# Kernel optimization log

Hardware: AMD Instinct MI355X
Metric: run time of the kernel (lower is better)

## Reference

```python
import jax, jax.numpy as jnp
import numpy as np
from jax import lax

ALIGNED_H = 7
ALIGNED_W = 7
SPATIAL_SCALE = 0.125
B, C, H, W = 4, 512, 96, 96
R = 512
IMG = 768  # image resolution (features are image/8)


def setup_inputs() -> dict:
    key = jax.random.key(0)
    k1, k2, k3, k4, k5, k6 = jax.random.split(key, 6)
    features = jax.random.normal(k1, (B, C, H, W), dtype=jnp.float32)
    # realistic rois: [batch_idx, x1, y1, x2, y2] in image coordinates
    bi = jax.random.randint(k2, (R,), 0, B).astype(jnp.float32)
    cx = jax.random.uniform(k3, (R,), minval=32.0, maxval=float(IMG - 32))
    cy = jax.random.uniform(k4, (R,), minval=32.0, maxval=float(IMG - 32))
    bw = jax.random.uniform(k5, (R,), minval=16.0, maxval=256.0)
    bh = jax.random.uniform(k6, (R,), minval=16.0, maxval=256.0)
    x1 = jnp.clip(cx - bw / 2, 0.0, IMG - 1.0)
    x2 = jnp.clip(cx + bw / 2, 0.0, IMG - 1.0)
    y1 = jnp.clip(cy - bh / 2, 0.0, IMG - 1.0)
    y2 = jnp.clip(cy + bh / 2, 0.0, IMG - 1.0)
    rois = jnp.stack([bi, x1, y1, x2, y2], axis=1)
    return {"features": features, "rois": rois}


def _roi_align_ada(features, rois, ah, aw, scale):
    """RoIAlignAda: per output pixel, average of a 3x3 adaptive-stride grid of
    bilinear samples centered at the bin point (RT-MDNet ROIAlignAdaForward)."""
    b, c, h, w = features.shape
    r = rois.shape[0]
    batch_ind = rois[:, 0].astype(jnp.int32)
    x1 = rois[:, 1] * scale
    y1 = rois[:, 2] * scale
    x2 = rois[:, 3] * scale
    y2 = rois[:, 4] * scale
    roi_w = jnp.maximum(x2 - x1, 0.0)
    roi_h = jnp.maximum(y2 - y1, 0.0)
    bin_h = roi_h / (ah - 1.0)  # [R]
    bin_w = roi_w / (aw - 1.0)
    ph = jnp.arange(ah, dtype=jnp.float32)
    pw = jnp.arange(aw, dtype=jnp.float32)
    hc = y1[:, None] + ph[None, :] * bin_h[:, None]  # [R, AH] bin centers
    wc = x1[:, None] + pw[None, :] * bin_w[:, None]  # [R, AW]
    stride_h = jnp.maximum(1.0, jnp.round(bin_h / 3.0))  # [R]
    stride_w = jnp.maximum(1.0, jnp.round(bin_w / 3.0))

    center_ok = ((hc >= 0) & (hc < h))[:, :, None] & ((wc >= 0) & (wc < w))[:, None, :]  # [R,AH,AW]

    # flatten spatial for gathers: [B*H*W, C]
    f = features.transpose(0, 2, 3, 1).reshape(b * h * w, c)
    base = batch_ind[:, None, None] * (h * w)  # [R,1,1]

    acc = jnp.zeros((r, ah, aw, c), dtype=features.dtype)
    cnt = jnp.zeros((r, ah, aw), dtype=features.dtype)
    for sh in (-1.0, 0.0, 1.0):
        for sw in (-1.0, 0.0, 1.0):
            ch = hc + sh * stride_h[:, None]  # [R,AH]
            cw = wc + sw * stride_w[:, None]  # [R,AW]
            valid = ((ch >= 0) & (ch < h))[:, :, None] & ((cw >= 0) & (cw < w))[:, None, :]
            hs = jnp.clip(jnp.floor(ch), 0.0, h - 2.0)
            ws = jnp.clip(jnp.floor(cw), 0.0, w - 2.0)
            hr = (ch - hs)[:, :, None]  # [R,AH,1]
            wr = (cw - ws)[:, None, :] * jnp.ones((r, ah, aw), features.dtype)[:, :1, :1]  # broadcast helper
            wr = (cw - ws)[:, None, :]  # [R,1,AW]
            hsi = hs.astype(jnp.int32)[:, :, None]  # [R,AH,1]
            wsi = ws.astype(jnp.int32)[:, None, :]  # [R,1,AW]
            ul = base + hsi * w + wsi  # [R,AH,AW]
            v = (f[ul] * ((1.0 - hr) * (1.0 - wr))[..., None]
                 + f[ul + 1] * ((1.0 - hr) * wr)[..., None]
                 + f[ul + w] * (hr * (1.0 - wr))[..., None]
                 + f[ul + w + 1] * (hr * wr)[..., None])  # [R,AH,AW,C]
            acc = acc + jnp.where(valid[..., None], v, 0.0)
            cnt = cnt + valid.astype(features.dtype)

    out = jnp.where(center_ok[..., None], acc / jnp.maximum(cnt, 1.0)[..., None], 0.0)
    return out.transpose(0, 3, 1, 2)  # [R, C, AH, AW]


def reference(features, rois):
    x = _roi_align_ada(features, rois, ALIGNED_H + 4, ALIGNED_W + 4, SPATIAL_SCALE)  # [R,C,11,11]
    # fused 3x3 stride-2 max pool -> [R, C, 5, 5]
    out = lax.reduce_window(x, -jnp.inf, lax.max,
                            window_dimensions=(1, 1, 3, 3),
                            window_strides=(1, 1, 2, 2),
                            padding='VALID')
    return out
```

## Files before the change

### kernel.cpp

```cpp
#include <hip/hip_runtime.h>
#include <stdint.h>

typedef unsigned short u16;
typedef unsigned int   u32;

#define Bn 4
#define Cc 512
#define Hh 96
#define Ww 96
#define HWc (Hh*Ww)
#define AH 11
#define Rr 512
#define CP (Cc/2)

__device__ __forceinline__ u16 f2bf(float f){
  u32 u = __float_as_uint(f);
  u += 0x7fffu + ((u>>16)&1u);
  return (u16)(u>>16);
}
__device__ __forceinline__ u32 pk2(float a, float b){
  return (u32)f2bf(a) | ((u32)f2bf(b)<<16);
}

__global__ __launch_bounds__(256)
void transpose_kernel(const float* __restrict__ in, u32* __restrict__ out,
                      const float* __restrict__ rois, int* __restrict__ idx){
  __shared__ u32 tile[128*64];
  const int t = threadIdx.x;
  const int hw0 = blockIdx.x*128, c0 = blockIdx.y*128, b = blockIdx.z;
  {
    const int q = t & 31, cp0 = t >> 5;
    const float* ib = in + ((size_t)(b*Cc + c0))*HWc + hw0 + 4*q;
    #pragma unroll
    for (int p=0;p<8;++p){
      const int cp = cp0 + p*8;
      const float* pa = ib + (size_t)(2*cp)*HWc;
      float4 A = *(const float4*)pa;
      float4 B = *(const float4*)(pa + HWc);
      const int cs = cp ^ q;
      tile[(4*q+0)*64 + cs] = pk2(A.x,B.x);
      tile[(4*q+1)*64 + cs] = pk2(A.y,B.y);
      tile[(4*q+2)*64 + cs] = pk2(A.z,B.z);
      tile[(4*q+3)*64 + cs] = pk2(A.w,B.w);
    }
  }
  __syncthreads();
  {
    const int l = t & 63, wv = t >> 6;
    const int rsub = l >> 4, q = l & 15;
    u32* ob = out + ((size_t)b*HWc + hw0)*CP + (c0>>1);
    #pragma unroll
    for (int k=0;k<8;++k){
      const int hw = wv*32 + k*4 + rsub;
      const int s  = hw >> 2;
      const int m  = s & 3;
      const u32* tp = &tile[hw*64 + ((4*q) ^ (s & ~3))];
      uint4 R = *(const uint4*)tp;
      uint4 W;
      if      (m==0) W = R;
      else if (m==1) W = make_uint4(R.y,R.x,R.w,R.z);
      else if (m==2) W = make_uint4(R.z,R.w,R.x,R.y);
      else           W = make_uint4(R.w,R.z,R.y,R.x);
      *(uint4*)(ob + (size_t)hw*CP + 4*q) = W;
    }
  }
  if (idx && blockIdx.x==0 && blockIdx.y==0 && blockIdx.z==0){
    __shared__ int cnt[4], off[4], cur[4];
    if (t < 4) cnt[t] = 0;
    __syncthreads();
    int b0 = min(max((int)rois[t*5], 0), Bn-1);
    int b1 = min(max((int)rois[(t+256)*5], 0), Bn-1);
    atomicAdd(&cnt[b0], 1);
    atomicAdd(&cnt[b1], 1);
    __syncthreads();
    if (t == 0){
      int o = 0;
      for (int i=0;i<4;++i){ off[i]=o; cur[i]=o; o+=cnt[i]; }
    }
    __syncthreads();
    int p0 = atomicAdd(&cur[b0], 1); idx[8+p0] = t;
    int p1 = atomicAdd(&cur[b1], 1); idx[8+p1] = t+256;
    if (t < 4){ idx[t] = cnt[t]; idx[4+t] = off[t]; }
  }
}

__device__ __forceinline__ float4 bilin2(const uint2 v[16], const float cw[4], const float rw[4]){
  float ax0=0.0f, ay0=0.0f, ax1=0.0f, ay1=0.0f;
  #pragma unroll
  for (int i=0;i<4;++i){
    float cx0=0.0f, cy0=0.0f, cx1=0.0f, cy1=0.0f;
    #pragma unroll
    for (int j=0;j<4;++j){
      uint2 d = v[i*4+j];
      float w = cw[j];
      cx0 = fmaf(w, __uint_as_float(d.x<<16),           cx0);
      cy0 = fmaf(w, __uint_as_float(d.x & 0xffff0000u), cy0);
      cx1 = fmaf(w, __uint_as_float(d.y<<16),           cx1);
      cy1 = fmaf(w, __uint_as_float(d.y & 0xffff0000u), cy1);
    }
    ax0 = fmaf(rw[i], cx0, ax0);
    ay0 = fmaf(rw[i], cy0, ay0);
    ax1 = fmaf(rw[i], cx1, ax1);
    ay1 = fmaf(rw[i], cy1, ay1);
  }
  return make_float4(ax0, ay0, ax1, ay1);
}

__global__ __launch_bounds__(64)
void roi_align_max_nhwc(const u32* __restrict__ feat,
                        const float* __restrict__ rois,
                        float* __restrict__ out,
                        const int* __restrict__ idx)
{
  __shared__ __align__(16) int4   s_ro[AH];
  __shared__ __align__(16) float4 s_rw[AH];
  __shared__ __align__(16) int4   s_co[AH];
  __shared__ __align__(16) float4 s_cw[AH];
  __shared__ int s_b;
  __shared__ __align__(16) float s_out[256*25];

  const int t   = threadIdx.x;
  const int bid = blockIdx.x;

  int r, half;
  if (idx){
    const int k = bid & 7;
    const int j = bid >> 3;
    const int b = k >> 1;
    half = k & 1;
    const int cntb = idx[b];
    if (j < cntb && j < 128){
      r = idx[8 + idx[4+b] + j];
    } else {
      int dr = 0;
      for (int b2=0; b2<b; ++b2) dr += max(0, 128 - idx[b2]);
      dr += j - min(cntb, 128);
      int acc = 0; r = 0;
      for (int b2=0; b2<4; ++b2){
        int ex = max(0, idx[b2] - 128);
        if (dr < acc + ex){ r = idx[8 + idx[4+b2] + 128 + (dr - acc)]; break; }
        acc += ex;
      }
    }
  } else {
    r = bid >> 1; half = bid & 1;
  }

  if (t == 0){
    int b = (int)rois[r*5+0];
    s_b = min(max(b, 0), Bn-1);
  }

  if (t < AH || (t >= 32 && t < 32+AH)){
    const bool isrow = (t < AH);
    const int  p = isrow ? t : t-32;
    const float* rp = rois + r*5;
    const float c1 = rp[isrow?2:1], c2 = rp[isrow?4:3];
    float lo  = __fmul_rn(c1, 0.125f);
    float hi  = __fmul_rn(c2, 0.125f);
    float ext = fmaxf(__fsub_rn(hi,lo), 0.0f);
    float bin = __fdiv_rn(ext, 10.0f);
    float ctr = __fadd_rn(lo, __fmul_rn((float)p, bin));
    float strd = fmaxf(1.0f, rintf(__fdiv_rn(bin, 3.0f)));
    bool ok = (ctr >= 0.0f) && (ctr < 96.0f);
    int rws[6]; float wts[6]; int nv=0;
    #pragma unroll
    for (int s=0;s<3;++s){
      float cc = __fadd_rn(ctr, __fmul_rn((float)(s-1), strd));
      bool vv = (cc >= 0.0f) && (cc < 96.0f);
      float fl = fminf(fmaxf(floorf(cc),0.0f),94.0f);
      float fr = __fsub_rn(cc, fl);
      int ri = (int)fl;
      rws[2*s]=ri; rws[2*s+1]=ri+1;
      wts[2*s]  = vv ? __fsub_rn(1.0f,fr) : 0.0f;
      wts[2*s+1]= vv ? fr : 0.0f;
      nv += vv?1:0;
    }
    float sc = ok ? (1.0f/(float)nv) : 0.0f;
    int cr[4]={0,0,0,0}; float cwv[4]={0.0f,0.0f,0.0f,0.0f}; int n=0;
    for (int k=0;k<6;++k){
      float wk=wts[k]; if (wk==0.0f) continue;
      int rr=rws[k]; bool fnd=false;
      for (int j=0;j<n;++j) if (cr[j]==rr){ cwv[j]+=wk; fnd=true; break; }
      if (!fnd && n<4){ cr[n]=rr; cwv[n]=wk; ++n; }
    }
    const int mul = isrow ? (Ww*CP*4) : (CP*4);
    if (isrow){
      s_ro[p] = make_int4(cr[0]*mul, cr[1]*mul, cr[2]*mul, cr[3]*mul);
      s_rw[p] = make_float4(cwv[0]*sc, cwv[1]*sc, cwv[2]*sc, cwv[3]*sc);
    } else {
      s_co[p] = make_int4(cr[0]*mul, cr[1]*mul, cr[2]*mul, cr[3]*mul);
      s_cw[p] = make_float4(cwv[0]*sc, cwv[1]*sc, cwv[2]*sc, cwv[3]*sc);
    }
  }
  __syncthreads();

  const int sb = __builtin_amdgcn_readfirstlane(s_b);
  const char* fb = (const char*)feat + (size_t)sb*((size_t)HWc*CP*4);
  const int tb4 = (half*128 + 2*t)*4;

  int   vo[AH][4]; float cwr[AH][4];
  #pragma unroll
  for (int pw=0; pw<AH; ++pw){
    int4 c4 = s_co[pw]; float4 w4 = s_cw[pw];
    vo[pw][0]=tb4+c4.x; vo[pw][1]=tb4+c4.y; vo[pw][2]=tb4+c4.z; vo[pw][3]=tb4+c4.w;
    cwr[pw][0]=w4.x; cwr[pw][1]=w4.y; cwr[pw][2]=w4.z; cwr[pw][3]=w4.w;
  }

  float4 awin[5];
  #pragma unroll 1
  for (int ph=0; ph<AH; ++ph){
    int4   r4 = s_ro[ph];
    float4 w4 = s_rw[ph];
    const char* r0 = fb + __builtin_amdgcn_readfirstlane(r4.x);
    const char* r1 = fb + __builtin_amdgcn_readfirstlane(r4.y);
    const char* r2 = fb + __builtin_amdgcn_readfirstlane(r4.z);
    const char* r3 = fb + __builtin_amdgcn_readfirstlane(r4.w);
    const float rw_[4] = {w4.x, w4.y, w4.z, w4.w};
    float4 binr[AH];
    uint2 va[16], vb[16], vc[16], vd[16];

#define LDV(dst, PW) do{                                \
    dst[ 0] = *(const uint2*)(r0 + vo[PW][0]);          \
    dst[ 1] = *(const uint2*)(r0 + vo[PW][1]);          \
    dst[ 2] = *(const uint2*)(r0 + vo[PW][2]);          \
    dst[ 3] = *(const uint2*)(r0 + vo[PW][3]);          \
    dst[ 4] = *(const uint2*)(r1 + vo[PW][0]);          \
    dst[ 5] = *(const uint2*)(r1 + vo[PW][1]);          \
    dst[ 6] = *(const uint2*)(r1 + vo[PW][2]);          \
    dst[ 7] = *(const uint2*)(r1 + vo[PW][3]);          \
    dst[ 8] = *(const uint2*)(r2 + vo[PW][0]);          \
    dst[ 9] = *(const uint2*)(r2 + vo[PW][1]);          \
    dst[10] = *(const uint2*)(r2 + vo[PW][2]);          \
    dst[11] = *(const uint2*)(r2 + vo[PW][3]);          \
    dst[12] = *(const uint2*)(r3 + vo[PW][0]);          \
    dst[13] = *(const uint2*)(r3 + vo[PW][1]);          \
    dst[14] = *(const uint2*)(r3 + vo[PW][2]);          \
    dst[15] = *(const uint2*)(r3 + vo[PW][3]);          \
  }while(0)
#define CMP(src, PW) binr[PW] = bilin2(src, cwr[PW], rw_)

    LDV(va, 0); LDV(vb, 1); LDV(vc, 2); LDV(vd, 3);
    CMP(va, 0); LDV(va, 4);
    CMP(vb, 1); LDV(vb, 5);
    CMP(vc, 2); LDV(vc, 6);
    CMP(vd, 3); LDV(vd, 7);
    CMP(va, 4); LDV(va, 8);
    CMP(vb, 5); LDV(vb, 9);
    CMP(vc, 6); LDV(vc, 10);
    CMP(vd, 7);
    CMP(va, 8);
    CMP(vb, 9);
    CMP(vc, 10);
#undef LDV
#undef CMP

    float4 rm[5];
    #pragma unroll
    for (int ox=0; ox<5; ++ox){
      rm[ox].x = fmaxf(fmaxf(binr[2*ox].x, binr[2*ox+1].x), binr[2*ox+2].x);
      rm[ox].y = fmaxf(fmaxf(binr[2*ox].y, binr[2*ox+1].y), binr[2*ox+2].y);
      rm[ox].z = fmaxf(fmaxf(binr[2*ox].z, binr[2*ox+1].z), binr[2*ox+2].z);
      rm[ox].w = fmaxf(fmaxf(binr[2*ox].w, binr[2*ox+1].w), binr[2*ox+2].w);
    }
    if (ph == 0){
      #pragma unroll
      for (int ox=0; ox<5; ++ox) awin[ox] = rm[ox];
    } else if (ph & 1){
      #pragma unroll
      for (int ox=0; ox<5; ++ox){
        awin[ox].x = fmaxf(awin[ox].x, rm[ox].x);
        awin[ox].y = fmaxf(awin[ox].y, rm[ox].y);
        awin[ox].z = fmaxf(awin[ox].z, rm[ox].z);
        awin[ox].w = fmaxf(awin[ox].w, rm[ox].w);
      }
    } else {
      const int oy = (ph-2) >> 1;
      #pragma unroll
      for (int ox=0; ox<5; ++ox){
        s_out[(4*t+0)*25 + oy*5 + ox] = fmaxf(awin[ox].x, rm[ox].x);
        s_out[(4*t+1)*25 + oy*5 + ox] = fmaxf(awin[ox].y, rm[ox].y);
        s_out[(4*t+2)*25 + oy*5 + ox] = fmaxf(awin[ox].z, rm[ox].z);
        s_out[(4*t+3)*25 + oy*5 + ox] = fmaxf(awin[ox].w, rm[ox].w);
        awin[ox] = rm[ox];
      }
    }
  }
  __syncthreads();

  float4* dst = (float4*)(out + (size_t)r*(Cc*25) + half*(256*25));
  const float4* src = (const float4*)s_out;
  for (int k=t; k<(256*25)/4; k+=64) dst[k]=src[k];
}

__global__ __launch_bounds__(512, 1)
void roi_align_max_nchw(const float* __restrict__ feat,
                        const float* __restrict__ rois,
                        float* __restrict__ out)
{
  __shared__ int   s_roff[AH][6];
  __shared__ float s_rw  [AH][6];
  __shared__ int   s_coff[AH][6];
  __shared__ float s_cw  [AH][6];
  __shared__ int   s_b;
  __shared__ __align__(16) float s_out[Cc*25];

  const int t = threadIdx.x;
  const int r = blockIdx.x;

  if (t < AH*6){
    ((float*)s_rw)[t] = 0.0f;  ((int*)s_roff)[t] = 0;
    ((float*)s_cw)[t] = 0.0f;  ((int*)s_coff)[t] = 0;
  }
  if (t == 0){
    int b = (int)rois[r*5+0];
    s_b = min(max(b, 0), Bn-1);
  }
  __syncthreads();

  if (t < AH || (t >= 64 && t < 64+AH)){
    const bool isrow = (t < AH);
    const int  p = isrow ? t : t-64;
    const float* rp = rois + r*5;
    const float c1 = rp[isrow?2:1], c2 = rp[isrow?4:3];
    float lo  = __fmul_rn(c1, 0.125f);
    float hi  = __fmul_rn(c2, 0.125f);
    float ext = fmaxf(__fsub_rn(hi,lo), 0.0f);
    float bin = __fdiv_rn(ext, 10.0f);
    float ctr = __fadd_rn(lo, __fmul_rn((float)p, bin));
    float strd = fmaxf(1.0f, rintf(__fdiv_rn(bin, 3.0f)));
    bool ok = (ctr >= 0.0f) && (ctr < 96.0f);
    int rws[6]; float wts[6]; int nv=0;
    #pragma unroll
    for (int s=0;s<3;++s){
      float cc = __fadd_rn(ctr, __fmul_rn((float)(s-1), strd));
      bool vv = (cc >= 0.0f) && (cc < 96.0f);
      float fl = fminf(fmaxf(floorf(cc),0.0f),94.0f);
      float fr = __fsub_rn(cc, fl);
      int ri = (int)fl;
      rws[2*s]=ri; rws[2*s+1]=ri+1;
      wts[2*s]  = vv ? __fsub_rn(1.0f,fr) : 0.0f;
      wts[2*s+1]= vv ? fr : 0.0f;
      nv += vv?1:0;
    }
    float sc = ok ? (1.0f/(float)nv) : 0.0f;
    int cr[6]; float cw[6]; int n=0;
    for (int k=0;k<6;++k){
      float wk=wts[k]; if (wk==0.0f) continue;
      if (n>0 && cr[n-1]==rws[k]) cw[n-1]+=wk;
      else { cr[n]=rws[k]; cw[n]=wk; ++n; }
    }
    const int mul = isrow ? Ww : 1;
    for (int k=0;k<n;++k){
      int off = cr[k]*mul;
      float wv = cw[k]*sc;
      if (isrow){ s_roff[p][k]=off; s_rw[p][k]=wv; }
      else      { s_coff[p][k]=off; s_cw[p][k]=wv; }
    }
  }
  __syncthreads();

  const float* f0 = feat + ((size_t)s_b*Cc + t)*HWc;
  float awin[5];
  for (int ph=0; ph<AH; ++ph){
    float binrow[AH];
    #pragma unroll
    for (int pw=0; pw<AH; ++pw){
      float acc = 0.0f;
      #pragma unroll
      for (int ai=0; ai<6; ++ai){
        float ra = s_rw[ph][ai];
        if (ra == 0.0f) continue;
        int ro = s_roff[ph][ai];
        #pragma unroll
        for (int bi=0; bi<6; ++bi){
          float cb = s_cw[pw][bi];
          if (cb == 0.0f) continue;
          acc = fmaf(ra*cb, f0[ro + s_coff[pw][bi]], acc);
        }
      }
      binrow[pw] = acc;
    }
    float rm[5];
    #pragma unroll
    for (int ox=0; ox<5; ++ox)
      rm[ox] = fmaxf(fmaxf(binrow[2*ox], binrow[2*ox+1]), binrow[2*ox+2]);
    if (ph == 0){
      #pragma unroll
      for (int ox=0; ox<5; ++ox) awin[ox] = rm[ox];
    } else if (ph & 1){
      #pragma unroll
      for (int ox=0; ox<5; ++ox) awin[ox] = fmaxf(awin[ox], rm[ox]);
    } else {
      int oy = (ph-2) >> 1;
      #pragma unroll
      for (int ox=0; ox<5; ++ox){
        s_out[t*25 + oy*5 + ox] = fmaxf(awin[ox], rm[ox]);
        awin[ox] = rm[ox];
      }
    }
  }
  __syncthreads();

  float4* dst = (float4*)(out + (size_t)r*(Cc*25));
  const float4* src = (const float4*)s_out;
  for (int k=t; k<(Cc*25)/4; k+=512) dst[k]=src[k];
}

extern "C" void kernel_launch(void* const* d_in, const int* in_sizes, int n_in,
                              void* d_out, int out_size, void* d_ws, size_t ws_size,
                              hipStream_t stream)
{
  (void)in_sizes; (void)n_in; (void)out_size;
  const float* feat = (const float*)d_in[0];
  const float* rois = (const float*)d_in[1];
  float* out = (float*)d_out;
  const size_t need = (size_t)Bn*HWc*Cc*sizeof(u16);
  if (ws_size >= need){
    u32* ws = (u32*)d_ws;
    int* idx = nullptr;
    if (ws_size >= need + 4096) idx = (int*)((char*)d_ws + need);
    dim3 g(HWc/128, Cc/128, Bn);
    transpose_kernel<<<g, 256, 0, stream>>>(feat, ws, rois, idx);
    roi_align_max_nhwc<<<Rr*2, 64, 0, stream>>>(ws, rois, out, idx);
  } else {
    roi_align_max_nchw<<<Rr, 512, 0, stream>>>(feat, rois, out);
  }
}
```

Before: 182.1 us.

## Split each RoI's output rows across two blocks to double grid parallelism

Each (RoI, channel-half) block is split into two row-groups: one computes aligned rows 0-6 (output rows 0-2), the other rows 6-10 (output rows 3-4). The grid doubles to 2048 blocks of 64 threads and the shared output buffer shrinks, which raises occupancy and parallelism on the many CUs. The cost is that row 6 is sampled by both blocks, the per-block setup is repeated, and the output stores become scalar and strided instead of float4.

Result: slower. 193.6 us (+6.3%).

```diff
diff --git a/kernel.cpp b/kernel.cpp
--- a/kernel.cpp
+++ b/kernel.cpp
@@ -117,24 +117,26 @@
   __shared__ __align__(16) int4   s_co[AH];
   __shared__ __align__(16) float4 s_cw[AH];
   __shared__ int s_b;
-  __shared__ __align__(16) float s_out[256*25];
+  __shared__ __align__(16) float s_out[256*15];
 
   const int t   = threadIdx.x;
   const int bid = blockIdx.x;
 
-  int r, half;
+  int r, half, rg;
   if (idx){
     const int k = bid & 7;
     const int j = bid >> 3;
     const int b = k >> 1;
     half = k & 1;
+    rg   = j >> 7;
+    const int jj = j & 127;
     const int cntb = idx[b];
-    if (j < cntb && j < 128){
-      r = idx[8 + idx[4+b] + j];
+    if (jj < cntb && jj < 128){
+      r = idx[8 + idx[4+b] + jj];
     } else {
       int dr = 0;
       for (int b2=0; b2<b; ++b2) dr += max(0, 128 - idx[b2]);
-      dr += j - min(cntb, 128);
+      dr += jj - min(cntb, 128);
       int acc = 0; r = 0;
       for (int b2=0; b2<4; ++b2){
         int ex = max(0, idx[b2] - 128);
@@ -143,7 +145,7 @@
       }
     }
   } else {
-    r = bid >> 1; half = bid & 1;
+    r = bid >> 2; half = (bid >> 1) & 1; rg = bid & 1;
   }
 
   if (t == 0){
@@ -181,7 +183,7 @@
     for (int k=0;k<6;++k){
       float wk=wts[k]; if (wk==0.0f) continue;
       int rr=rws[k]; bool fnd=false;
-      for (int j=0;j<n;++j) if (cr[j]==rr){ cwv[j]+=wk; fnd=true; break; }
+      for (int j2=0;j2<n;++j2) if (cr[j2]==rr){ cwv[j2]+=wk; fnd=true; break; }
       if (!fnd && n<4){ cr[n]=rr; cwv[n]=wk; ++n; }
     }
     const int mul = isrow ? (Ww*CP*4) : (CP*4);
@@ -208,8 +210,11 @@
   }
 
   float4 awin[5];
+  const int ph0 = rg ? 6 : 0;
+  const int phN = rg ? 10 : 6;
+  const int oyb = rg ? 3 : 0;
   #pragma unroll 1
-  for (int ph=0; ph<AH; ++ph){
+  for (int ph=ph0; ph<=phN; ++ph){
     int4   r4 = s_ro[ph];
     float4 w4 = s_rw[ph];
     const char* r0 = fb + __builtin_amdgcn_readfirstlane(r4.x);
@@ -263,7 +268,7 @@
       rm[ox].z = fmaxf(fmaxf(binr[2*ox].z, binr[2*ox+1].z), binr[2*ox+2].z);
       rm[ox].w = fmaxf(fmaxf(binr[2*ox].w, binr[2*ox+1].w), binr[2*ox+2].w);
     }
-    if (ph == 0){
+    if (ph == ph0){
       #pragma unroll
       for (int ox=0; ox<5; ++ox) awin[ox] = rm[ox];
     } else if (ph & 1){
@@ -275,22 +280,31 @@
         awin[ox].w = fmaxf(awin[ox].w, rm[ox].w);
       }
     } else {
-      const int oy = (ph-2) >> 1;
+      const int oy = ((ph-2) >> 1) - oyb;
       #pragma unroll
       for (int ox=0; ox<5; ++ox){
-        s_out[(4*t+0)*25 + oy*5 + ox] = fmaxf(awin[ox].x, rm[ox].x);
-        s_out[(4*t+1)*25 + oy*5 + ox] = fmaxf(awin[ox].y, rm[ox].y);
-        s_out[(4*t+2)*25 + oy*5 + ox] = fmaxf(awin[ox].z, rm[ox].z);
-        s_out[(4*t+3)*25 + oy*5 + ox] = fmaxf(awin[ox].w, rm[ox].w);
+        s_out[(4*t+0)*15 + oy*5 + ox] = fmaxf(awin[ox].x, rm[ox].x);
+        s_out[(4*t+1)*15 + oy*5 + ox] = fmaxf(awin[ox].y, rm[ox].y);
+        s_out[(4*t+2)*15 + oy*5 + ox] = fmaxf(awin[ox].z, rm[ox].z);
+        s_out[(4*t+3)*15 + oy*5 + ox] = fmaxf(awin[ox].w, rm[ox].w);
         awin[ox] = rm[ox];
       }
     }
   }
   __syncthreads();
 
-  float4* dst = (float4*)(out + (size_t)r*(Cc*25) + half*(256*25));
-  const float4* src = (const float4*)s_out;
-  for (int k=t; k<(256*25)/4; k+=64) dst[k]=src[k];
+  float* ob = out + (size_t)r*(Cc*25) + half*(256*25);
+  if (rg == 0){
+    for (int k=t; k<256*15; k+=64){
+      int c = k/15, e = k - c*15;
+      ob[c*25 + e] = s_out[k];
+    }
+  } else {
+    for (int k=t; k<256*10; k+=64){
+      int c = k/10, e = k - c*10;
+      ob[c*25 + 15 + e] = s_out[c*15 + e];
+    }
+  }
 }
 
 __global__ __launch_bounds__(512, 1)
@@ -422,7 +436,7 @@
     if (ws_size >= need + 4096) idx = (int*)((char*)d_ws + need);
     dim3 g(HWc/128, Cc/128, Bn);
     transpose_kernel<<<g, 256, 0, stream>>>(feat, ws, rois, idx);
-    roi_align_max_nhwc<<<Rr*2, 64, 0, stream>>>(ws, rois, out, idx);
+    roi_align_max_nhwc<<<Rr*4, 64, 0, stream>>>(ws, rois, out, idx);
   } else {
     roi_align_max_nchw<<<Rr, 512, 0, stream>>>(feat, rois, out);
   }
```
